# Performance work log

Measured on AMD Instinct MI355X. Metric: run time of the kernel, lower is better.

Reference implementation:

```python
import jax, jax.numpy as jnp
import numpy as np

N, E, D = 50000, 800000, 256

def setup_inputs() -> dict:
    key = jax.random.key(0)
    ks = jax.random.split(key, 12)
    s = 1.0 / np.sqrt(D)
    return {
        "x": jax.random.normal(ks[0], (N, D), dtype=jnp.float32),
        "src": jax.random.randint(ks[1], (E,), 0, N, dtype=jnp.int64),
        "dst": jax.random.randint(ks[2], (E,), 0, N, dtype=jnp.int64),
        "W_w": jax.random.normal(ks[3], (D, D), dtype=jnp.float32) * s,
        "W_b": jnp.zeros((D,), dtype=jnp.float32),
        "U_w": jax.random.normal(ks[4], (D, D), dtype=jnp.float32) * s,
        "U_b": jnp.zeros((D,), dtype=jnp.float32),
        "V_w": jax.random.normal(ks[5], (D, D), dtype=jnp.float32) * s,
        "V_b": jnp.zeros((D,), dtype=jnp.float32),
        "attn_l": jax.random.normal(ks[6], (D,), dtype=jnp.float32) * s,
        "attn_r": jax.random.normal(ks[7], (D,), dtype=jnp.float32) * s,
        "gamma": jnp.ones((D,), dtype=jnp.float32),
        "beta": jnp.zeros((D,), dtype=jnp.float32),
    }

def reference(x, src, dst, W_w, W_b, U_w, U_b, V_w, V_b, attn_l, attn_r, gamma, beta):
    # node transforms (dropout p=0 -> identity)
    Wh = x @ W_w + W_b            # [N, D]
    Uh = x @ U_w + U_b            # [N, D]
    Vh = x @ V_w + V_b            # [N, D]
    out_src = Wh * attn_l         # [N, D]
    out_dst = Wh * attn_r         # [N, D]
    # per-edge gate: sigma = sigmoid(out_src[u] + out_dst[v])  [E, D]
    sigma = jax.nn.sigmoid(out_src[src] + out_dst[dst])
    # aggregate to destination nodes
    sum_sigma_h = jax.ops.segment_sum(Vh[src] * sigma, dst, num_segments=N)
    sum_sigma = jax.ops.segment_sum(sigma, dst, num_segments=N)
    h = Uh + sum_sigma_h / (sum_sigma + 1e-6)
    # layer norm (eps=1e-6, affine)
    mu = jnp.mean(h, axis=-1, keepdims=True)
    var = jnp.mean((h - mu) ** 2, axis=-1, keepdims=True)
    h = (h - mu) / jnp.sqrt(var + 1e-6) * gamma + beta
    h = jax.nn.relu(h)
    return x + h  # residual
```

## Files before the change

kernel.cpp:

```cpp
#include <hip/hip_runtime.h>
#include <hip/hip_bf16.h>

#define NN 50000
#define NE 800000
#define NB 196
#define NROWPAD 50048

#define XCVT_BLOCKS 6250
#define TW_BLOCKS   192
#define HIST_BLOCKS 3125

#if __has_builtin(__builtin_amdgcn_cvt_pk_fp8_f32) && __has_builtin(__builtin_amdgcn_cvt_pk_f32_fp8)
#define HAVE_FP8 1
#define ROWB 768
#else
#define HAVE_FP8 0
#define ROWB 1024
#endif

typedef __attribute__((ext_vector_type(8))) short short8;
typedef __attribute__((ext_vector_type(4))) float floatx4;
typedef __attribute__((ext_vector_type(2))) float floatx2;
typedef unsigned short u16;
typedef unsigned int u32;

__device__ __forceinline__ u16 f2bf(float f) {
    u32 u = __float_as_uint(f);
    u += 0x7FFFu + ((u >> 16) & 1u);
    return (u16)(u >> 16);
}
__device__ __forceinline__ float bf_lo(u32 u) { return __uint_as_float(u << 16); }
__device__ __forceinline__ float bf_hi(u32 u) { return __uint_as_float(u & 0xFFFF0000u); }
__device__ __forceinline__ u32 pack_bf(float lo, float hi) {
    return (u32)f2bf(lo) | ((u32)f2bf(hi) << 16);
}
__device__ __forceinline__ void gl_lds16(const void* g, void* l) {
    __builtin_amdgcn_global_load_lds((const __attribute__((address_space(1))) void*)g,
                                     (__attribute__((address_space(3))) void*)l, 16, 0, 0);
}

#if __has_builtin(__builtin_amdgcn_exp2f)
#define EXP2F(x) __builtin_amdgcn_exp2f(x)
#else
#define EXP2F(x) exp2f(x)
#endif

__global__ __launch_bounds__(256) void prep_kernel(
    const float* __restrict__ x, u16* __restrict__ xbf,
    const float* __restrict__ W, const float* __restrict__ U, const float* __restrict__ V,
    u16* __restrict__ wT, const int* __restrict__ dst, int* __restrict__ deg, int do_xcvt) {
    __shared__ float s[32][33];
    int b = blockIdx.x;
    int xb = do_xcvt ? XCVT_BLOCKS : 0;
    if (b < xb) {
        size_t i = ((size_t)b * 256 + threadIdx.x) * 8;
        floatx4 f0 = *(const floatx4*)(x + i);
        floatx4 f1 = *(const floatx4*)(x + i + 4);
        uint4 pk;
        pk.x = pack_bf(f0[0], f0[1]);
        pk.y = pack_bf(f0[2], f0[3]);
        pk.z = pack_bf(f1[0], f1[1]);
        pk.w = pack_bf(f1[2], f1[3]);
        *(uint4*)(xbf + i) = pk;
    } else if (b < xb + TW_BLOCKS) {
        int bb = b - xb;
        int g = bb >> 6, rem = bb & 63;
        int r0 = (rem & 7) * 32, c0 = (rem >> 3) * 32;
        const float* M = (g == 0) ? W : ((g == 1) ? U : V);
        int tx = threadIdx.x & 31, ty = threadIdx.x >> 5;
#pragma unroll
        for (int k = 0; k < 4; ++k)
            s[ty + k * 8][tx] = M[(size_t)(r0 + ty + k * 8) * 256 + c0 + tx];
        __syncthreads();
#pragma unroll
        for (int k = 0; k < 4; ++k)
            wT[(size_t)(g * 256 + c0 + ty + k * 8) * 256 + r0 + tx] = f2bf(s[tx][ty + k * 8]);
    } else {
        int e = (b - xb - TW_BLOCKS) * 256 + threadIdx.x;
        if (e < NE) atomicAdd(&deg[dst[e]], 1);
    }
}

__global__ __launch_bounds__(256) void scanA_kernel(const int* __restrict__ deg, int* __restrict__ bsum) {
    int t = threadIdx.x;
    int i = blockIdx.x * 256 + t;
    int v = (i < NN) ? deg[i] : 0;
#pragma unroll
    for (int m = 32; m; m >>= 1) v += __shfl_xor(v, m, 64);
    __shared__ int ws[4];
    if ((t & 63) == 0) ws[t >> 6] = v;
    __syncthreads();
    if (t == 0) bsum[blockIdx.x] = ws[0] + ws[1] + ws[2] + ws[3];
}

__global__ __launch_bounds__(256) void scanB_kernel(const int* __restrict__ bsum, int* __restrict__ bpre,
                                                    int* __restrict__ rows_end) {
    int t = threadIdx.x, lane = t & 63, wv = t >> 6;
    int v = (t < NB) ? bsum[t] : 0;
    int inc = v;
#pragma unroll
    for (int off = 1; off < 64; off <<= 1) {
        int u = __shfl_up(inc, off, 64);
        if (lane >= off) inc += u;
    }
    __shared__ int wsum[4];
    if (lane == 63) wsum[wv] = inc;
    __syncthreads();
    int woff = 0;
    for (int k = 0; k < wv; ++k) woff += wsum[k];
    if (t < NB) bpre[t] = woff + inc - v;
    if (t == 255) rows_end[0] = woff + inc;
}

__global__ __launch_bounds__(256) void scanC_kernel(const int* __restrict__ deg, const int* __restrict__ bpre,
                                                    int* __restrict__ rows, int* __restrict__ cursor) {
    int t = threadIdx.x, lane = t & 63, wv = t >> 6;
    int i = blockIdx.x * 256 + t;
    int v = (i < NN) ? deg[i] : 0;
    int inc = v;
#pragma unroll
    for (int off = 1; off < 64; off <<= 1) {
        int u = __shfl_up(inc, off, 64);
        if (lane >= off) inc += u;
    }
    __shared__ int wsum[4];
    if (lane == 63) wsum[wv] = inc;
    __syncthreads();
    int woff = bpre[blockIdx.x];
    for (int k = 0; k < wv; ++k) woff += wsum[k];
    int excl = woff + inc - v;
    if (i < NN) { rows[i] = excl; cursor[i] = excl; }
}

__global__ void scatter_kernel(const int* __restrict__ src, const int* __restrict__ dst,
                               int* __restrict__ cursor, int* __restrict__ esrc) {
    int e = blockIdx.x * 256 + threadIdx.x;
    if (e < NE) {
        int d = dst[e];
        int pos = atomicAdd(&cursor[d], 1);
        esrc[pos] = src[e];
    }
}

template<bool USE_BF>
__global__ __launch_bounds__(512, 2) void gemm8_kernel(
    const u16* __restrict__ xbf, const float* __restrict__ xf, const u16* __restrict__ wT,
    const float* __restrict__ Wb, const float* __restrict__ Ub, const float* __restrict__ Vb,
    char* __restrict__ WVh, float* __restrict__ Uh) {
    __shared__ __align__(16) u16 Bs[256 * 256];

    int rb = blockIdx.x * 256;
    int pass = blockIdx.y;
    int cbg = pass * 256;

    int t = threadIdx.x, lane = t & 63, w = t >> 6;

#pragma unroll
    for (int i = 0; i < 16; ++i) {
        int slot = w * 16 + i;
        int ci = slot * 2 + (lane >> 5);
        int q = (lane & 31) ^ (ci & 7);
        gl_lds16(wT + (size_t)(cbg + ci) * 256 + q * 8, Bs + slot * 512);
    }

    int arow0 = rb + w * 32 + (lane & 15);
    short8 afr[2][8];
    if (USE_BF) {
#pragma unroll
        for (int rg = 0; rg < 2; ++rg) {
            int row = min(arow0 + rg * 16, NN - 1);
            const u16* p = xbf + (size_t)row * 256 + (lane >> 4) * 8;
#pragma unroll
            for (int ks = 0; ks < 8; ++ks)
                afr[rg][ks] = *(const short8*)(p + ks * 32);
        }
    } else {
#pragma unroll
        for (int rg = 0; rg < 2; ++rg) {
            int row = min(arow0 + rg * 16, NN - 1);
            const float* p = xf + (size_t)row * 256 + (lane >> 4) * 8;
#pragma unroll
            for (int ks = 0; ks < 8; ++ks) {
                floatx4 f0 = *(const floatx4*)(p + ks * 32);
                floatx4 f1 = *(const floatx4*)(p + ks * 32 + 4);
                uint4 pk;
                pk.x = pack_bf(f0[0], f0[1]);
                pk.y = pack_bf(f0[2], f0[3]);
                pk.z = pack_bf(f1[0], f1[1]);
                pk.w = pack_bf(f1[2], f1[3]);
                afr[rg][ks] = *(short8*)&pk;
            }
        }
    }
    __syncthreads();

    floatx4 acc[2][16] = {};
#pragma unroll
    for (int ks = 0; ks < 8; ++ks) {
#pragma unroll
        for (int cf = 0; cf < 16; ++cf) {
            int ci = cf * 16 + (lane & 15);
            int q = (ks * 4 + (lane >> 4)) ^ (ci & 7);
            short8 bfrag = *(const short8*)(Bs + ci * 256 + q * 8);
            acc[0][cf] = __builtin_amdgcn_mfma_f32_16x16x32_bf16(bfrag, afr[0][ks], acc[0][cf], 0, 0, 0);
            acc[1][cf] = __builtin_amdgcn_mfma_f32_16x16x32_bf16(bfrag, afr[1][ks], acc[1][cf], 0, 0, 0);
        }
    }

    const float* bias = (pass == 0) ? Wb : ((pass == 1) ? Ub : Vb);
#pragma unroll
    for (int rg = 0; rg < 2; ++rg) {
        int noderow = rb + w * 32 + rg * 16 + (lane & 15);
        if (noderow >= NN) continue;
#pragma unroll
        for (int cf = 0; cf < 16; ++cf) {
            int colc = cf * 16 + (lane >> 4) * 4;
            floatx4 bv = *(const floatx4*)(bias + colc);
            float v0 = acc[rg][cf][0] + bv[0];
            float v1 = acc[rg][cf][1] + bv[1];
            float v2 = acc[rg][cf][2] + bv[2];
            float v3 = acc[rg][cf][3] + bv[3];
            if (pass == 1) {
                floatx4 o = { v0, v1, v2, v3 };
                *(floatx4*)(Uh + (size_t)noderow * 256 + colc) = o;
            } else if (pass == 0) {
#if HAVE_FP8
                u32 p = 0;
                p = __builtin_amdgcn_cvt_pk_fp8_f32(v0, v1, p, false);
                p = __builtin_amdgcn_cvt_pk_fp8_f32(v2, v3, p, true);
                *(u32*)(WVh + (size_t)noderow * ROWB + colc) = p;
#else
                uint2 o = { pack_bf(v0, v1), pack_bf(v2, v3) };
                *(uint2*)(WVh + (size_t)noderow * ROWB + colc * 2) = o;
#endif
            } else {
#if HAVE_FP8
                uint2 o = { pack_bf(v0, v1), pack_bf(v2, v3) };
                *(uint2*)(WVh + (size_t)noderow * ROWB + 256 + colc * 2) = o;
#else
                uint2 o = { pack_bf(v0, v1), pack_bf(v2, v3) };
                *(uint2*)(WVh + (size_t)noderow * ROWB + 512 + colc * 2) = o;
#endif
            }
        }
    }
}

__global__ __launch_bounds__(256) void node_kernel(
    const char* __restrict__ WVh, const float* __restrict__ x,
    const int* __restrict__ rows, const int* __restrict__ esrc,
    const float* __restrict__ attn_l, const float* __restrict__ attn_r,
    const float* __restrict__ gamma, const float* __restrict__ beta,
    float* inout) {
    int wv = threadIdx.x >> 6, lane = threadIdx.x & 63;
    int v = blockIdx.x * 4 + wv;
    if (v >= NN) return;
    int c0 = lane * 4;

    const float NL2E = -1.44269504f;
    floatx4 alv = *(const floatx4*)(attn_l + c0);
    floatx4 arv = *(const floatx4*)(attn_r + c0);

    float mywf[4];
#if HAVE_FP8
    {
        u32 myw = *(const u32*)(WVh + (size_t)v * ROWB + lane * 4);
        floatx2 a = __builtin_amdgcn_cvt_pk_f32_fp8(myw, false);
        floatx2 b = __builtin_amdgcn_cvt_pk_f32_fp8(myw, true);
        mywf[0] = a[0]; mywf[1] = a[1]; mywf[2] = b[0]; mywf[3] = b[1];
    }
#else
    {
        uint2 myw = *(const uint2*)(WVh + (size_t)v * ROWB + lane * 8);
        mywf[0] = bf_lo(myw.x); mywf[1] = bf_hi(myw.x);
        mywf[2] = bf_lo(myw.y); mywf[3] = bf_hi(myw.y);
    }
#endif
    float al2[4] = { alv[0] * NL2E, alv[1] * NL2E, alv[2] * NL2E, alv[3] * NL2E };
    float td2[4] = { mywf[0] * arv[0] * NL2E, mywf[1] * arv[1] * NL2E,
                     mywf[2] * arv[2] * NL2E, mywf[3] * arv[3] * NL2E };

    float acc_h[4] = {0.f, 0.f, 0.f, 0.f};
    float acc_s[4] = {0.f, 0.f, 0.f, 0.f};

#if HAVE_FP8
    auto edge = [&](u32 w8, uint2 vu) {
        floatx2 a = __builtin_amdgcn_cvt_pk_f32_fp8(w8, false);
        floatx2 b = __builtin_amdgcn_cvt_pk_f32_fp8(w8, true);
        float wf[4] = { a[0], a[1], b[0], b[1] };
        float vf[4] = { bf_lo(vu.x), bf_hi(vu.x), bf_lo(vu.y), bf_hi(vu.y) };
#pragma unroll
        for (int j = 0; j < 4; ++j) {
            float m = fmaf(wf[j], al2[j], td2[j]);
            float s = __builtin_amdgcn_rcpf(1.0f + EXP2F(m));
            acc_s[j] += s;
            acc_h[j] = fmaf(s, vf[j], acc_h[j]);
        }
    };
    int e = rows[v], e1 = rows[v + 1];
    for (; e + 8 <= e1; e += 8) {
        int us[8];
#pragma unroll
        for (int q = 0; q < 8; ++q) us[q] = esrc[e + q];
        u32 w8[8]; uint2 vu[8];
#pragma unroll
        for (int q = 0; q < 8; ++q) {
            const char* p = WVh + (size_t)us[q] * ROWB;
            w8[q] = *(const u32*)(p + lane * 4);
            vu[q] = *(const uint2*)(p + 256 + lane * 8);
        }
#pragma unroll
        for (int q = 0; q < 8; ++q) edge(w8[q], vu[q]);
    }
    for (; e < e1; ++e) {
        const char* p = WVh + (size_t)esrc[e] * ROWB;
        edge(*(const u32*)(p + lane * 4), *(const uint2*)(p + 256 + lane * 8));
    }
#else
    auto edge = [&](uint2 wu, uint2 vu) {
        float wf[4] = { bf_lo(wu.x), bf_hi(wu.x), bf_lo(wu.y), bf_hi(wu.y) };
        float vf[4] = { bf_lo(vu.x), bf_hi(vu.x), bf_lo(vu.y), bf_hi(vu.y) };
#pragma unroll
        for (int j = 0; j < 4; ++j) {
            float m = fmaf(wf[j], al2[j], td2[j]);
            float s = __builtin_amdgcn_rcpf(1.0f + EXP2F(m));
            acc_s[j] += s;
            acc_h[j] = fmaf(s, vf[j], acc_h[j]);
        }
    };
    int e = rows[v], e1 = rows[v + 1];
    for (; e + 8 <= e1; e += 8) {
        int us[8];
#pragma unroll
        for (int q = 0; q < 8; ++q) us[q] = esrc[e + q];
        uint2 wu[8], vu[8];
#pragma unroll
        for (int q = 0; q < 8; ++q) {
            const char* p = WVh + (size_t)us[q] * ROWB;
            wu[q] = *(const uint2*)(p + lane * 8);
            vu[q] = *(const uint2*)(p + 512 + lane * 8);
        }
#pragma unroll
        for (int q = 0; q < 8; ++q) edge(wu[q], vu[q]);
    }
    for (; e < e1; ++e) {
        const char* p = WVh + (size_t)esrc[e] * ROWB;
        edge(*(const uint2*)(p + lane * 8), *(const uint2*)(p + 512 + lane * 8));
    }
#endif

    floatx4 uh = *(const floatx4*)(inout + (size_t)v * 256 + c0);
    float h[4];
#pragma unroll
    for (int j = 0; j < 4; ++j)
        h[j] = uh[j] + acc_h[j] * __builtin_amdgcn_rcpf(acc_s[j] + 1e-6f);

    float s01 = h[0] + h[1] + h[2] + h[3];
#pragma unroll
    for (int m = 32; m; m >>= 1) s01 += __shfl_xor(s01, m, 64);
    float mu = s01 * (1.0f / 256.0f);
    float d[4] = { h[0] - mu, h[1] - mu, h[2] - mu, h[3] - mu };
    float sq = d[0] * d[0] + d[1] * d[1] + d[2] * d[2] + d[3] * d[3];
#pragma unroll
    for (int m = 32; m; m >>= 1) sq += __shfl_xor(sq, m, 64);
    float inv = rsqrtf(sq * (1.0f / 256.0f) + 1e-6f);

    floatx4 gm = *(const floatx4*)(gamma + c0);
    floatx4 bt = *(const floatx4*)(beta + c0);
    floatx4 xr = *(const floatx4*)(x + (size_t)v * 256 + c0);
    floatx4 res;
#pragma unroll
    for (int j = 0; j < 4; ++j) {
        float y = d[j] * inv * gm[j] + bt[j];
        y = fmaxf(y, 0.0f);
        res[j] = xr[j] + y;
    }
    *(floatx4*)(inout + (size_t)v * 256 + c0) = res;
}

extern "C" void kernel_launch(void* const* d_in, const int* in_sizes, int n_in,
                              void* d_out, int out_size, void* d_ws, size_t ws_size,
                              hipStream_t stream) {
    const float* x       = (const float*)d_in[0];
    const int*   src     = (const int*)d_in[1];
    const int*   dst     = (const int*)d_in[2];
    const float* W_w     = (const float*)d_in[3];
    const float* W_b     = (const float*)d_in[4];
    const float* U_w     = (const float*)d_in[5];
    const float* U_b     = (const float*)d_in[6];
    const float* V_w     = (const float*)d_in[7];
    const float* V_b     = (const float*)d_in[8];
    const float* attn_l  = (const float*)d_in[9];
    const float* attn_r  = (const float*)d_in[10];
    const float* gamma   = (const float*)d_in[11];
    const float* beta    = (const float*)d_in[12];

    char* ws = (char*)d_ws;
    size_t off = 0;
    auto alloc = [&](size_t bytes) -> char* {
        char* p = ws + off;
        off += (bytes + 255) & ~(size_t)255;
        return p;
    };
    char* WVh    = alloc((size_t)NN * ROWB);
    u16* wT      = (u16*)alloc((size_t)768 * 256 * 2);
    int* deg     = (int*)alloc((size_t)NN * 4);
    int* rows    = (int*)alloc((size_t)(NN + 1) * 4);
    int* cursor  = (int*)alloc((size_t)NN * 4);
    int* esrc    = (int*)alloc((size_t)NE * 4);
    int* bsum    = (int*)alloc((size_t)NB * 4);
    int* bpre    = (int*)alloc((size_t)NB * 4);
    u16* xbf     = (u16*)alloc((size_t)NROWPAD * 256 * 2);
    bool use_bf  = (ws_size >= off);

    float* Uh_f32 = (float*)d_out;

    hipMemsetAsync(deg, 0, (size_t)NN * 4, stream);

    int xb = use_bf ? XCVT_BLOCKS : 0;
    prep_kernel<<<xb + TW_BLOCKS + HIST_BLOCKS, 256, 0, stream>>>(
        x, xbf, W_w, U_w, V_w, wT, dst, deg, use_bf ? 1 : 0);

    scanA_kernel<<<NB, 256, 0, stream>>>(deg, bsum);
    scanB_kernel<<<1, 256, 0, stream>>>(bsum, bpre, rows + NN);
    scanC_kernel<<<NB, 256, 0, stream>>>(deg, bpre, rows, cursor);
    scatter_kernel<<<(NE + 255) / 256, 256, 0, stream>>>(src, dst, cursor, esrc);

    dim3 gg(NB, 3);
    if (use_bf) {
        gemm8_kernel<true><<<gg, 512, 0, stream>>>(xbf, x, wT, W_b, U_b, V_b, WVh, Uh_f32);
    } else {
        gemm8_kernel<false><<<gg, 512, 0, stream>>>(nullptr, x, wT, W_b, U_b, V_b, WVh, Uh_f32);
    }

    node_kernel<<<(NN + 3) / 4, 256, 0, stream>>>(
        WVh, x, rows, esrc, attn_l, attn_r, gamma, beta, (float*)d_out);
}
```

Measured before the change: 273.2 us.

## Fuse CSR build into cooperative kernel and retile GEMM with XCD-aware mapping

The four CSR-construction launches (block sums, top-level scan, per-block scan, edge scatter) are merged into one cooperative kernel that uses grid-wide syncs, falling back to the separate kernels if the cooperative launch fails. This removes launch gaps between small kernels. The GEMM is retiled to 1024-thread blocks, each covering 256 rows and 128 output columns with 64KB of LDS. The 1D grid of 1176 blocks is remapped so that consecutive work groups on the same XCD share row tiles of x. The risks are grid-sync overhead, a scatter phase that now runs on only 196 blocks, and lower per-block MFMA reuse in the GEMM.

Measured after the change: 334.3 us. 22.3% more time.

```diff
diff --git a/kernel.cpp b/kernel.cpp
--- a/kernel.cpp
+++ b/kernel.cpp
@@ -1,5 +1,8 @@
 #include <hip/hip_runtime.h>
 #include <hip/hip_bf16.h>
+#include <hip/hip_cooperative_groups.h>
+
+namespace cg = cooperative_groups;
 
 #define NN 50000
 #define NE 800000
@@ -9,6 +12,7 @@
 #define XCVT_BLOCKS 6250
 #define TW_BLOCKS   192
 #define HIST_BLOCKS 3125
+#define GEMM_BLOCKS 1176
 
 #if __has_builtin(__builtin_amdgcn_cvt_pk_fp8_f32) && __has_builtin(__builtin_amdgcn_cvt_pk_f32_fp8)
 #define HAVE_FP8 1
@@ -81,6 +85,69 @@
     }
 }
 
+__global__ __launch_bounds__(256) void graph_kernel(
+    const int* __restrict__ deg, int* __restrict__ bsum, int* __restrict__ bpre,
+    int* __restrict__ rows, int* __restrict__ cursor,
+    const int* __restrict__ src, const int* __restrict__ dst, int* __restrict__ esrc) {
+    cg::grid_group grid = cg::this_grid();
+    int t = threadIdx.x, lane = t & 63, wv = t >> 6;
+    __shared__ int wsum[4];
+
+    {
+        int i = blockIdx.x * 256 + t;
+        int v = (i < NN) ? deg[i] : 0;
+#pragma unroll
+        for (int m = 32; m; m >>= 1) v += __shfl_xor(v, m, 64);
+        if (lane == 0) wsum[wv] = v;
+        __syncthreads();
+        if (t == 0) bsum[blockIdx.x] = wsum[0] + wsum[1] + wsum[2] + wsum[3];
+        __syncthreads();
+    }
+    grid.sync();
+
+    if (blockIdx.x == 0) {
+        int v = (t < NB) ? bsum[t] : 0;
+        int inc = v;
+#pragma unroll
+        for (int off = 1; off < 64; off <<= 1) {
+            int u = __shfl_up(inc, off, 64);
+            if (lane >= off) inc += u;
+        }
+        if (lane == 63) wsum[wv] = inc;
+        __syncthreads();
+        int woff = 0;
+        for (int k = 0; k < wv; ++k) woff += wsum[k];
+        if (t < NB) bpre[t] = woff + inc - v;
+        if (t == 255) rows[NN] = woff + inc;
+    }
+    grid.sync();
+
+    {
+        int i = blockIdx.x * 256 + t;
+        int v = (i < NN) ? deg[i] : 0;
+        int inc = v;
+#pragma unroll
+        for (int off = 1; off < 64; off <<= 1) {
+            int u = __shfl_up(inc, off, 64);
+            if (lane >= off) inc += u;
+        }
+        __syncthreads();
+        if (lane == 63) wsum[wv] = inc;
+        __syncthreads();
+        int woff = bpre[blockIdx.x];
+        for (int k = 0; k < wv; ++k) woff += wsum[k];
+        int excl = woff + inc - v;
+        if (i < NN) { rows[i] = excl; cursor[i] = excl; }
+    }
+    grid.sync();
+
+    for (int e = blockIdx.x * 256 + t; e < NE; e += NB * 256) {
+        int d = dst[e];
+        int pos = atomicAdd(&cursor[d], 1);
+        esrc[pos] = src[e];
+    }
+}
+
 __global__ __launch_bounds__(256) void scanA_kernel(const int* __restrict__ deg, int* __restrict__ bsum) {
     int t = threadIdx.x;
     int i = blockIdx.x * 256 + t;
@@ -92,7 +159,6 @@
     __syncthreads();
     if (t == 0) bsum[blockIdx.x] = ws[0] + ws[1] + ws[2] + ws[3];
 }
-
 __global__ __launch_bounds__(256) void scanB_kernel(const int* __restrict__ bsum, int* __restrict__ bpre,
                                                     int* __restrict__ rows_end) {
     int t = threadIdx.x, lane = t & 63, wv = t >> 6;
@@ -111,7 +177,6 @@
     if (t < NB) bpre[t] = woff + inc - v;
     if (t == 255) rows_end[0] = woff + inc;
 }
-
 __global__ __launch_bounds__(256) void scanC_kernel(const int* __restrict__ deg, const int* __restrict__ bpre,
                                                     int* __restrict__ rows, int* __restrict__ cursor) {
     int t = threadIdx.x, lane = t & 63, wv = t >> 6;
@@ -131,7 +196,6 @@
     int excl = woff + inc - v;
     if (i < NN) { rows[i] = excl; cursor[i] = excl; }
 }
-
 __global__ void scatter_kernel(const int* __restrict__ src, const int* __restrict__ dst,
                                int* __restrict__ cursor, int* __restrict__ esrc) {
     int e = blockIdx.x * 256 + threadIdx.x;
@@ -143,105 +207,98 @@
 }
 
 template<bool USE_BF>
-__global__ __launch_bounds__(512, 2) void gemm8_kernel(
+__global__ __launch_bounds__(1024, 1) void gemm11_kernel(
     const u16* __restrict__ xbf, const float* __restrict__ xf, const u16* __restrict__ wT,
     const float* __restrict__ Wb, const float* __restrict__ Ub, const float* __restrict__ Vb,
     char* __restrict__ WVh, float* __restrict__ Uh) {
-    __shared__ __align__(16) u16 Bs[256 * 256];
-
-    int rb = blockIdx.x * 256;
-    int pass = blockIdx.y;
-    int cbg = pass * 256;
+    __shared__ __align__(16) u16 Bs[128 * 256];
+
+    int B = blockIdx.x;
+    int xcd = B & 7, j = B >> 3;
+    int wgid = xcd * 147 + j;
+    int bx = wgid / 6, cg6 = wgid % 6;
+    int rb = bx * 256;
+    int cbg = cg6 * 128;
 
     int t = threadIdx.x, lane = t & 63, w = t >> 6;
 
 #pragma unroll
-    for (int i = 0; i < 16; ++i) {
-        int slot = w * 16 + i;
+    for (int i = 0; i < 4; ++i) {
+        int slot = w * 4 + i;
         int ci = slot * 2 + (lane >> 5);
         int q = (lane & 31) ^ (ci & 7);
         gl_lds16(wT + (size_t)(cbg + ci) * 256 + q * 8, Bs + slot * 512);
     }
 
-    int arow0 = rb + w * 32 + (lane & 15);
-    short8 afr[2][8];
+    int arow = rb + w * 16 + (lane & 15);
+    int rowc = min(arow, NN - 1);
+    short8 afr[8];
     if (USE_BF) {
-#pragma unroll
-        for (int rg = 0; rg < 2; ++rg) {
-            int row = min(arow0 + rg * 16, NN - 1);
-            const u16* p = xbf + (size_t)row * 256 + (lane >> 4) * 8;
-#pragma unroll
-            for (int ks = 0; ks < 8; ++ks)
-                afr[rg][ks] = *(const short8*)(p + ks * 32);
-        }
+        const u16* p = xbf + (size_t)rowc * 256 + (lane >> 4) * 8;
+#pragma unroll
+        for (int ks = 0; ks < 8; ++ks)
+            afr[ks] = *(const short8*)(p + ks * 32);
     } else {
-#pragma unroll
-        for (int rg = 0; rg < 2; ++rg) {
-            int row = min(arow0 + rg * 16, NN - 1);
-            const float* p = xf + (size_t)row * 256 + (lane >> 4) * 8;
-#pragma unroll
-            for (int ks = 0; ks < 8; ++ks) {
-                floatx4 f0 = *(const floatx4*)(p + ks * 32);
-                floatx4 f1 = *(const floatx4*)(p + ks * 32 + 4);
-                uint4 pk;
-                pk.x = pack_bf(f0[0], f0[1]);
-                pk.y = pack_bf(f0[2], f0[3]);
-                pk.z = pack_bf(f1[0], f1[1]);
-                pk.w = pack_bf(f1[2], f1[3]);
-                afr[rg][ks] = *(short8*)&pk;
-            }
+        const float* p = xf + (size_t)rowc * 256 + (lane >> 4) * 8;
+#pragma unroll
+        for (int ks = 0; ks < 8; ++ks) {
+            floatx4 f0 = *(const floatx4*)(p + ks * 32);
+            floatx4 f1 = *(const floatx4*)(p + ks * 32 + 4);
+            uint4 pk;
+            pk.x = pack_bf(f0[0], f0[1]);
+            pk.y = pack_bf(f0[2], f0[3]);
+            pk.z = pack_bf(f1[0], f1[1]);
+            pk.w = pack_bf(f1[2], f1[3]);
+            afr[ks] = *(short8*)&pk;
         }
     }
     __syncthreads();
 
-    floatx4 acc[2][16] = {};
+    floatx4 acc[8] = {};
 #pragma unroll
     for (int ks = 0; ks < 8; ++ks) {
 #pragma unroll
-        for (int cf = 0; cf < 16; ++cf) {
+        for (int cf = 0; cf < 8; ++cf) {
             int ci = cf * 16 + (lane & 15);
             int q = (ks * 4 + (lane >> 4)) ^ (ci & 7);
             short8 bfrag = *(const short8*)(Bs + ci * 256 + q * 8);
-            acc[0][cf] = __builtin_amdgcn_mfma_f32_16x16x32_bf16(bfrag, afr[0][ks], acc[0][cf], 0, 0, 0);
-            acc[1][cf] = __builtin_amdgcn_mfma_f32_16x16x32_bf16(bfrag, afr[1][ks], acc[1][cf], 0, 0, 0);
-        }
-    }
-
-    const float* bias = (pass == 0) ? Wb : ((pass == 1) ? Ub : Vb);
-#pragma unroll
-    for (int rg = 0; rg < 2; ++rg) {
-        int noderow = rb + w * 32 + rg * 16 + (lane & 15);
-        if (noderow >= NN) continue;
-#pragma unroll
-        for (int cf = 0; cf < 16; ++cf) {
-            int colc = cf * 16 + (lane >> 4) * 4;
-            floatx4 bv = *(const floatx4*)(bias + colc);
-            float v0 = acc[rg][cf][0] + bv[0];
-            float v1 = acc[rg][cf][1] + bv[1];
-            float v2 = acc[rg][cf][2] + bv[2];
-            float v3 = acc[rg][cf][3] + bv[3];
-            if (pass == 1) {
-                floatx4 o = { v0, v1, v2, v3 };
-                *(floatx4*)(Uh + (size_t)noderow * 256 + colc) = o;
-            } else if (pass == 0) {
+            acc[cf] = __builtin_amdgcn_mfma_f32_16x16x32_bf16(bfrag, afr[ks], acc[cf], 0, 0, 0);
+        }
+    }
+
+    if (arow >= NN) return;
+    int g = cg6 >> 1;
+    int cloc = (cg6 & 1) * 128;
+    const float* bias = (g == 0) ? Wb : ((g == 1) ? Ub : Vb);
+#pragma unroll
+    for (int cf = 0; cf < 8; ++cf) {
+        int colc = cloc + cf * 16 + (lane >> 4) * 4;
+        floatx4 bv = *(const floatx4*)(bias + colc);
+        float v0 = acc[cf][0] + bv[0];
+        float v1 = acc[cf][1] + bv[1];
+        float v2 = acc[cf][2] + bv[2];
+        float v3 = acc[cf][3] + bv[3];
+        if (g == 1) {
+            floatx4 o = { v0, v1, v2, v3 };
+            *(floatx4*)(Uh + (size_t)arow * 256 + colc) = o;
+        } else if (g == 0) {
 #if HAVE_FP8
-                u32 p = 0;
-                p = __builtin_amdgcn_cvt_pk_fp8_f32(v0, v1, p, false);
-                p = __builtin_amdgcn_cvt_pk_fp8_f32(v2, v3, p, true);
-                *(u32*)(WVh + (size_t)noderow * ROWB + colc) = p;
+            u32 p = 0;
+            p = __builtin_amdgcn_cvt_pk_fp8_f32(v0, v1, p, false);
+            p = __builtin_amdgcn_cvt_pk_fp8_f32(v2, v3, p, true);
+            *(u32*)(WVh + (size_t)arow * ROWB + colc) = p;
 #else
-                uint2 o = { pack_bf(v0, v1), pack_bf(v2, v3) };
-                *(uint2*)(WVh + (size_t)noderow * ROWB + colc * 2) = o;
+            uint2 o = { pack_bf(v0, v1), pack_bf(v2, v3) };
+            *(uint2*)(WVh + (size_t)arow * ROWB + colc * 2) = o;
 #endif
-            } else {
+        } else {
 #if HAVE_FP8
-                uint2 o = { pack_bf(v0, v1), pack_bf(v2, v3) };
-                *(uint2*)(WVh + (size_t)noderow * ROWB + 256 + colc * 2) = o;
+            uint2 o = { pack_bf(v0, v1), pack_bf(v2, v3) };
+            *(uint2*)(WVh + (size_t)arow * ROWB + 256 + colc * 2) = o;
 #else
-                uint2 o = { pack_bf(v0, v1), pack_bf(v2, v3) };
-                *(uint2*)(WVh + (size_t)noderow * ROWB + 512 + colc * 2) = o;
+            uint2 o = { pack_bf(v0, v1), pack_bf(v2, v3) };
+            *(uint2*)(WVh + (size_t)arow * ROWB + 512 + colc * 2) = o;
 #endif
-            }
         }
     }
 }
@@ -421,16 +478,23 @@
     prep_kernel<<<xb + TW_BLOCKS + HIST_BLOCKS, 256, 0, stream>>>(
         x, xbf, W_w, U_w, V_w, wT, dst, deg, use_bf ? 1 : 0);
 
-    scanA_kernel<<<NB, 256, 0, stream>>>(deg, bsum);
-    scanB_kernel<<<1, 256, 0, stream>>>(bsum, bpre, rows + NN);
-    scanC_kernel<<<NB, 256, 0, stream>>>(deg, bpre, rows, cursor);
-    scatter_kernel<<<(NE + 255) / 256, 256, 0, stream>>>(src, dst, cursor, esrc);
-
-    dim3 gg(NB, 3);
+    {
+        void* gargs[] = { (void*)&deg, (void*)&bsum, (void*)&bpre, (void*)&rows,
+                          (void*)&cursor, (void*)&src, (void*)&dst, (void*)&esrc };
+        hipError_t cerr = hipLaunchCooperativeKernel((void*)graph_kernel, dim3(NB), dim3(256),
+                                                     gargs, 0, stream);
+        if (cerr != hipSuccess) {
+            scanA_kernel<<<NB, 256, 0, stream>>>(deg, bsum);
+            scanB_kernel<<<1, 256, 0, stream>>>(bsum, bpre, rows + NN);
+            scanC_kernel<<<NB, 256, 0, stream>>>(deg, bpre, rows, cursor);
+            scatter_kernel<<<(NE + 255) / 256, 256, 0, stream>>>(src, dst, cursor, esrc);
+        }
+    }
+
     if (use_bf) {
-        gemm8_kernel<true><<<gg, 512, 0, stream>>>(xbf, x, wT, W_b, U_b, V_b, WVh, Uh_f32);
+        gemm11_kernel<true><<<GEMM_BLOCKS, 1024, 0, stream>>>(xbf, x, wT, W_b, U_b, V_b, WVh, Uh_f32);
     } else {
-        gemm8_kernel<false><<<gg, 512, 0, stream>>>(nullptr, x, wT, W_b, U_b, V_b, WVh, Uh_f32);
+        gemm11_kernel<false><<<GEMM_BLOCKS, 1024, 0, stream>>>(nullptr, x, wT, W_b, U_b, V_b, WVh, Uh_f32);
     }
 
     node_kernel<<<(NN + 3) / 4, 256, 0, stream>>>(
```
